# Performance work log

Measured on AMD Instinct MI355X. Metric: run time of the kernel, lower is better.

## Reference

```python
import jax, jax.numpy as jnp
import numpy as np

N = 50000
E = 800000
F_IN = 128
HEADS = 8
HID = 16
CLASSES = 40
NEG_SLOPE = 0.2


def setup_inputs() -> dict:
    key = jax.random.key(0)
    ks = jax.random.split(key, 10)
    return {
        "x": jax.random.normal(ks[0], (N, F_IN), jnp.float32),
        "edge_index": jax.random.randint(ks[1], (2, E), 0, N, jnp.int64),
        "W1": jax.random.normal(ks[2], (F_IN, HEADS * HID), jnp.float32) * 0.1,
        "a_src1": jax.random.normal(ks[3], (HEADS, HID), jnp.float32) * 0.1,
        "a_dst1": jax.random.normal(ks[4], (HEADS, HID), jnp.float32) * 0.1,
        "b1": jax.random.normal(ks[5], (HEADS * HID,), jnp.float32) * 0.1,
        "W2": jax.random.normal(ks[6], (HEADS * HID, CLASSES), jnp.float32) * 0.1,
        "a_src2": jax.random.normal(ks[7], (1, CLASSES), jnp.float32) * 0.1,
        "a_dst2": jax.random.normal(ks[8], (1, CLASSES), jnp.float32) * 0.1,
        "b2": jax.random.normal(ks[9], (CLASSES,), jnp.float32) * 0.1,
    }


def gat_conv(x, src, dst, W, a_src, a_dst, bias, heads, out_ch, concat):
    # x: [N, in] -> h: [N, H, C]
    h = (x @ W).reshape(N, heads, out_ch)
    e_src = jnp.einsum("nhc,hc->nh", h, a_src)  # [N, H]
    e_dst = jnp.einsum("nhc,hc->nh", h, a_dst)
    alpha = e_src[src] + e_dst[dst]             # [E, H]
    alpha = jax.nn.leaky_relu(alpha, NEG_SLOPE)
    # segment softmax over incoming edges of each dst node
    amax = jax.ops.segment_max(alpha, dst, num_segments=N)
    alpha = jnp.exp(alpha - amax[dst])
    denom = jax.ops.segment_sum(alpha, dst, num_segments=N)
    alpha = alpha / (denom[dst] + 1e-16)
    msg = h[src] * alpha[:, :, None]            # [E, H, C]
    out = jax.ops.segment_sum(msg, dst, num_segments=N)  # [N, H, C]
    out = out.reshape(N, heads * out_ch) if concat else out.mean(axis=1)
    return out + bias


def reference(x, edge_index, W1, a_src1, a_dst1, b1, W2, a_src2, a_dst2, b2):
    # PyG GATConv adds self-loops by default
    loops = jnp.arange(N, dtype=edge_index.dtype)
    src = jnp.concatenate([edge_index[0], loops])
    dst = jnp.concatenate([edge_index[1], loops])
    # inference: dropout layers are identity
    h = gat_conv(x, src, dst, W1, a_src1, a_dst1, b1, HEADS, HID, concat=True)
    h = jax.nn.elu(h)
    out = gat_conv(h, src, dst, W2, a_src2, a_dst2, b2, 1, CLASSES, concat=False)
    return out
```

## Files before the change

kernel.cpp:

```cpp
#include <hip/hip_runtime.h>
#include <math.h>

#define NN 50000
#define EE 800000
#define ET (EE + NN)
#define F_IN 128
#define HEADS 8
#define HID 16
#define C1 (HEADS * HID)
#define CLASSES 40
#define NEG_SLOPE 0.2f
#define LOG2E 1.4426950408889634f

#define NCHUNKS ((NN + 1023) / 1024)
#define NHIST 64
#define EPB (EE / NHIST)
#define LHN 25088
#define GB ((NN + 63) / 64)

typedef __attribute__((ext_vector_type(8))) short bf16x8;
typedef __attribute__((ext_vector_type(4))) float f32x4;
typedef __attribute__((ext_vector_type(8))) _Float16 h16x8;
typedef __attribute__((ext_vector_type(2))) _Float16 h16x2;

__device__ __forceinline__ unsigned cvtpk(float a, float b) {
    unsigned r;
    asm("v_cvt_pk_bf16_f32 %0, %1, %2" : "=v"(r) : "v"(a), "v"(b));
    return r;
}
__device__ __forceinline__ float fexp2(float x) {
    float r;
    asm("v_exp_f32 %0, %1\n\ts_nop 0" : "=v"(r) : "v"(x));
    return r;
}
__device__ __forceinline__ float bflo(unsigned u) { return __uint_as_float(u << 16); }
__device__ __forceinline__ float bfhi(unsigned u) { return __uint_as_float(u & 0xffff0000u); }
__device__ __forceinline__ float lrelu(float a) { return fmaxf(a, NEG_SLOPE * a); }
__device__ __forceinline__ unsigned short bf1(float a) { return (unsigned short)cvtpk(a, a); }
__device__ __forceinline__ float bf1f(float a) { return bflo(cvtpk(a, a)); }
__device__ __forceinline__ bf16x8 pack8(float f0, float f1, float f2, float f3,
                                        float f4, float f5, float f6, float f7) {
    union { unsigned u[4]; bf16x8 v; } U;
    U.u[0] = cvtpk(f0, f1);
    U.u[1] = cvtpk(f2, f3);
    U.u[2] = cvtpk(f4, f5);
    U.u[3] = cvtpk(f6, f7);
    return U.v;
}

__global__ void prep_kernel(const float* __restrict__ W1,
                            const float* __restrict__ as1, const float* __restrict__ ad1,
                            const float* __restrict__ W2,
                            const float* __restrict__ as2, const float* __restrict__ ad2,
                            const int* __restrict__ ei,
                            unsigned short* __restrict__ va1h, unsigned short* __restrict__ va1l,
                            unsigned short* __restrict__ va2b,
                            unsigned short* __restrict__ W1b, unsigned short* __restrict__ W2b,
                            unsigned* __restrict__ partial) {
    const int tid = threadIdx.x;
    const int b = blockIdx.x;
    if (b >= 3) {
        __shared__ unsigned lhist[LHN];
        for (int i = tid; i < LHN; i += 256) lhist[i] = 0;
        __syncthreads();
        const int hb = b - 3;
        const int* dp = ei + EE + hb * EPB;
        for (int e0 = tid * 4; e0 < EPB; e0 += 1024) {
            int4 d4 = *(const int4*)(dp + e0);
            atomicAdd(&lhist[(unsigned)d4.x >> 1], 1u << ((d4.x & 1) << 4));
            atomicAdd(&lhist[(unsigned)d4.y >> 1], 1u << ((d4.y & 1) << 4));
            atomicAdd(&lhist[(unsigned)d4.z >> 1], 1u << ((d4.z & 1) << 4));
            atomicAdd(&lhist[(unsigned)d4.w >> 1], 1u << ((d4.w & 1) << 4));
        }
        __syncthreads();
        unsigned* pb = partial + (size_t)hb * LHN;
        for (int i = tid; i < LHN; i += 256) pb[i] = lhist[i];
        return;
    }
    if (b == 1) {
        for (int f = tid; f < 2048; f += 256) {
            const int lane = f & 63, kc = (f >> 6) & 3, ntw = f >> 8;
            const int q = lane >> 4, c = lane & 15;
            const int col = ntw * 16 + c;
            const int k0 = kc * 32 + q * 8;
            const float* wp = W1 + (size_t)k0 * C1 + col;
            *(bf16x8*)(W1b + (size_t)f * 8) =
                pack8(wp[0], wp[C1], wp[2 * C1], wp[3 * C1],
                      wp[4 * C1], wp[5 * C1], wp[6 * C1], wp[7 * C1]);
        }
        return;
    }
    if (b == 2) {
        for (int f = tid; f < 768; f += 256) {
            const int lane = f & 63, kc = (f >> 6) & 3, nt = f >> 8;
            const int q = lane >> 4, c = lane & 15;
            const int col = nt * 16 + c;
            const int k0 = kc * 32 + q * 8;
            bf16x8 v = 0;
            if (col < CLASSES) {
                const float* wp = W2 + (size_t)k0 * CLASSES + col;
                v = pack8(wp[0], wp[CLASSES], wp[2 * CLASSES], wp[3 * CLASSES],
                          wp[4 * CLASSES], wp[5 * CLASSES], wp[6 * CLASSES], wp[7 * CLASSES]);
            }
            *(bf16x8*)(W2b + (size_t)f * 8) = v;
        }
        return;
    }
    {
        const int k = tid >> 1, half = tid & 1;
        const float* wrow = W1 + (size_t)k * C1 + half * 64;
        #pragma unroll
        for (int hh = 0; hh < 4; ++hh) {
            const int h = half * 4 + hh;
            float s = 0.f, d = 0.f;
            #pragma unroll
            for (int t = 0; t < 16; ++t) {
                float wv = wrow[hh * 16 + t];
                s += wv * as1[h * HID + t];
                d += wv * ad1[h * HID + t];
            }
            s *= LOG2E; d *= LOG2E;
            va1h[h * 128 + k]       = bf1(s);
            va1l[h * 128 + k]       = bf1(s - bf1f(s));
            va1h[(h + 8) * 128 + k] = bf1(d);
            va1l[(h + 8) * 128 + k] = bf1(d - bf1f(d));
        }
    }
    if (tid < C1) {
        const float* wrow = W2 + (size_t)tid * CLASSES;
        float s = 0.f, d = 0.f;
        #pragma unroll
        for (int c2 = 0; c2 < CLASSES; ++c2) {
            float wv = wrow[c2];
            s += wv * as2[c2];
            d += wv * ad2[c2];
        }
        s *= LOG2E; d *= LOG2E;
        va2b[0 * 128 + tid] = bf1(s);
        va2b[1 * 128 + tid] = bf1(s - bf1f(s));
        va2b[2 * 128 + tid] = bf1(d);
        va2b[3 * 128 + tid] = bf1(d - bf1f(d));
    }
}

__global__ void scan1_kernel(const unsigned* __restrict__ partial, int* __restrict__ deg,
                             int* __restrict__ rowptr, int* __restrict__ bsum) {
    __shared__ int sh[256];
    const int tid = threadIdx.x;
    const int base = blockIdx.x * 1024 + tid * 4;
    const unsigned short* pu = (const unsigned short*)partial;
    int t0 = 0, t1 = 0, t2 = 0, t3 = 0;
    #pragma unroll 8
    for (int b = 0; b < NHIST; ++b) {
        ushort4 p = *(const ushort4*)(pu + (size_t)b * (LHN * 2) + base);
        t0 += p.x; t1 += p.y; t2 += p.z; t3 += p.w;
    }
    int v[4], s[4];
    v[0] = (base + 0 < NN) ? t0 + 1 : 0;
    v[1] = (base + 1 < NN) ? t1 + 1 : 0;
    v[2] = (base + 2 < NN) ? t2 + 1 : 0;
    v[3] = (base + 3 < NN) ? t3 + 1 : 0;
    #pragma unroll
    for (int j = 0; j < 4; ++j)
        if (base + j < NN) deg[base + j] = v[j];
    s[0] = v[0]; s[1] = s[0] + v[1]; s[2] = s[1] + v[2]; s[3] = s[2] + v[3];
    int T = s[3];
    sh[tid] = T;
    __syncthreads();
    for (int off = 1; off < 256; off <<= 1) {
        int xv = (tid >= off) ? sh[tid - off] : 0;
        __syncthreads();
        sh[tid] += xv;
        __syncthreads();
    }
    int excl = sh[tid] - T;
    #pragma unroll
    for (int j = 0; j < 4; ++j)
        if (base + j < NN) rowptr[base + j] = excl + s[j] - v[j];
    if (tid == 255) bsum[blockIdx.x] = sh[255];
}

__global__ void scan3_kernel(int* __restrict__ rowptr, const int* __restrict__ bsum,
                             int* __restrict__ cursor, unsigned short* __restrict__ csr) {
    __shared__ int ex[64];
    const int tid = threadIdx.x;
    if (tid < 64) {
        int v = (tid < NCHUNKS) ? bsum[tid] : 0;
        int s = v;
        #pragma unroll
        for (int off = 1; off < 64; off <<= 1) {
            int xv = __shfl_up(s, off);
            if (tid >= off) s += xv;
        }
        ex[tid] = s - v;
    }
    __syncthreads();
    int i = blockIdx.x * blockDim.x + tid;
    if (i >= NN) return;
    int rp = rowptr[i] + ex[i >> 10];
    rowptr[i] = rp;
    cursor[i] = rp + 1;
    csr[rp] = (unsigned short)i;
}

__global__ __launch_bounds__(256, 4)
void gemm1_fill_kernel(const float* __restrict__ x,
                       const unsigned short* __restrict__ W1b,
                       const unsigned short* __restrict__ va1h,
                       const unsigned short* __restrict__ va1l,
                       const int* __restrict__ ei,
                       int* __restrict__ cursor, unsigned short* __restrict__ csr,
                       _Float16* __restrict__ h1h,
                       float* __restrict__ e_src, float* __restrict__ e_dst) {
    const int bid = blockIdx.x;
    const int tid = threadIdx.x;
    if (bid & 1) {
        int base = ((bid >> 1) * 256 + tid) * 4;
        if (base < EE) {
            int4 s4 = *(const int4*)(ei + base);
            int4 d4 = *(const int4*)(ei + EE + base);
            int p0 = atomicAdd(&cursor[d4.x], 1);
            int p1 = atomicAdd(&cursor[d4.y], 1);
            int p2 = atomicAdd(&cursor[d4.z], 1);
            int p3 = atomicAdd(&cursor[d4.w], 1);
            csr[p0] = (unsigned short)s4.x;
            csr[p1] = (unsigned short)s4.y;
            csr[p2] = (unsigned short)s4.z;
            csr[p3] = (unsigned short)s4.w;
        }
        return;
    }
    const int gemmb = bid >> 1;
    const int w = tid >> 6, lane = tid & 63;
    const int q = lane >> 4, c = lane & 15;
    const int m0 = (gemmb * 4 + w) * 16;

    int row = m0 + c;
    if (row > NN - 1) row = NN - 1;
    bf16x8 afrag[4];
    #pragma unroll
    for (int kc = 0; kc < 4; ++kc) {
        const float* xp = x + (size_t)row * F_IN + kc * 32 + q * 8;
        float4 p0 = *(const float4*)xp;
        float4 p1 = *(const float4*)(xp + 4);
        afrag[kc] = pack8(p0.x, p0.y, p0.z, p0.w, p1.x, p1.y, p1.z, p1.w);
    }

    {
        f32x4 acce = {0.f, 0.f, 0.f, 0.f};
        #pragma unroll
        for (int kc = 0; kc < 4; ++kc) {
            const int coloff = kc * 32 + q * 8;
            bf16x8 beh = *(const bf16x8*)(va1h + c * 128 + coloff);
            bf16x8 bel = *(const bf16x8*)(va1l + c * 128 + coloff);
            acce = __builtin_amdgcn_mfma_f32_16x16x32_bf16(afrag[kc], beh, acce, 0, 0, 0);
            acce = __builtin_amdgcn_mfma_f32_16x16x32_bf16(afrag[kc], bel, acce, 0, 0, 0);
        }
        float* ep = (c < 8) ? e_src : e_dst;
        const int cc = c & 7;
        #pragma unroll
        for (int r = 0; r < 4; ++r) {
            const int ro = m0 + q * 4 + r;
            if (ro < NN) ep[(size_t)ro * HEADS + cc] = acce[r];
        }
    }

    #pragma unroll 2
    for (int nt = 0; nt < 8; ++nt) {
        bf16x8 bf0 = *(const bf16x8*)(W1b + (size_t)((nt * 4 + 0) * 64 + lane) * 8);
        bf16x8 bf1_ = *(const bf16x8*)(W1b + (size_t)((nt * 4 + 1) * 64 + lane) * 8);
        bf16x8 bf2 = *(const bf16x8*)(W1b + (size_t)((nt * 4 + 2) * 64 + lane) * 8);
        bf16x8 bf3 = *(const bf16x8*)(W1b + (size_t)((nt * 4 + 3) * 64 + lane) * 8);
        f32x4 a = {0.f, 0.f, 0.f, 0.f};
        a = __builtin_amdgcn_mfma_f32_16x16x32_bf16(afrag[0], bf0, a, 0, 0, 0);
        a = __builtin_amdgcn_mfma_f32_16x16x32_bf16(afrag[1], bf1_, a, 0, 0, 0);
        a = __builtin_amdgcn_mfma_f32_16x16x32_bf16(afrag[2], bf2, a, 0, 0, 0);
        a = __builtin_amdgcn_mfma_f32_16x16x32_bf16(afrag[3], bf3, a, 0, 0, 0);
        #pragma unroll
        for (int r = 0; r < 4; ++r) {
            const int ro = m0 + q * 4 + r;
            if (ro < NN) h1h[(size_t)ro * C1 + nt * 16 + c] = (_Float16)a[r];
        }
    }
}

__global__ __launch_bounds__(64)
void agg1_kernel(const _Float16* __restrict__ h1h,
                 const float* __restrict__ e_src, const float* __restrict__ e_dst,
                 const int* __restrict__ rowptr, const int* __restrict__ deg,
                 const unsigned short* __restrict__ csr,
                 const float* __restrict__ b1, unsigned short* __restrict__ hmid) {
    const int tid = threadIdx.x;
    const int l = tid & 15;
    const int d = blockIdx.x * 4 + (tid >> 4);
    const int hd = l >> 1;
    const float ed = e_dst[(size_t)d * HEADS + hd];
    const int start = rowptr[d];
    const int cnt = deg[d];

    float denom = 0.f;
    float acc[8] = {0.f, 0.f, 0.f, 0.f, 0.f, 0.f, 0.f, 0.f};

    for (int i = 0; i < cnt; i += 8) {
        int s[8];
        #pragma unroll
        for (int e = 0; e < 8; ++e)
            s[e] = csr[start + ((i + e < cnt) ? i + e : i)];
        float es[8];
        #pragma unroll
        for (int e = 0; e < 8; ++e)
            es[e] = e_src[(size_t)s[e] * HEADS + hd];
        h16x8 g[8];
        #pragma unroll
        for (int e = 0; e < 8; ++e)
            g[e] = *(const h16x8*)(h1h + (size_t)s[e] * C1 + 8 * l);
        float w[8];
        #pragma unroll
        for (int e = 0; e < 8; ++e) {
            float we = fexp2(lrelu(es[e] + ed));
            w[e] = (i + e < cnt) ? we : 0.f;
            denom += w[e];
        }
        #pragma unroll
        for (int e = 0; e < 8; ++e) {
            #pragma unroll
            for (int j = 0; j < 8; ++j)
                acc[j] = fmaf((float)g[e][j], w[e], acc[j]);
        }
    }
    const float inv = 1.f / (denom + 1e-16f);
    float o[8];
    #pragma unroll
    for (int k = 0; k < 8; ++k) {
        float t = acc[k] * inv + b1[8 * l + k];
        o[k] = (t > 0.f) ? t : fexp2(t * LOG2E) - 1.f;
    }
    uint4 st;
    st.x = cvtpk(o[0], o[1]);
    st.y = cvtpk(o[2], o[3]);
    st.z = cvtpk(o[4], o[5]);
    st.w = cvtpk(o[6], o[7]);
    *(uint4*)(hmid + (size_t)d * C1 + 8 * l) = st;
}

__global__ __launch_bounds__(256, 4)
void gemm2_kernel(const unsigned short* __restrict__ hmid,
                  const unsigned short* __restrict__ W2b,
                  const unsigned short* __restrict__ va2b,
                  _Float16* __restrict__ h2h,
                  float* __restrict__ e_src, float* __restrict__ e_dst) {
    const int tid = threadIdx.x;
    const int w = tid >> 6, lane = tid & 63;
    const int q = lane >> 4, c = lane & 15;

    const int m0 = (blockIdx.x * 4 + w) * 16;
    if (m0 >= NN) return;
    int row = m0 + c;
    if (row > NN - 1) row = NN - 1;
    bf16x8 afrag[4];
    #pragma unroll
    for (int kc = 0; kc < 4; ++kc)
        afrag[kc] = *(const bf16x8*)(hmid + (size_t)row * C1 + kc * 32 + q * 8);

    bf16x8 bfrag[3][4];
    #pragma unroll
    for (int nt = 0; nt < 3; ++nt)
        #pragma unroll
        for (int kc = 0; kc < 4; ++kc)
            bfrag[nt][kc] = *(const bf16x8*)(W2b + (size_t)((nt * 4 + kc) * 64 + lane) * 8);
    bf16x8 bfe[4];
    #pragma unroll
    for (int kc = 0; kc < 4; ++kc) {
        bf16x8 bb = 0;
        if (c < 4) bb = *(const bf16x8*)(va2b + c * 128 + kc * 32 + q * 8);
        bfe[kc] = bb;
    }

    f32x4 acc[3] = {{0.f,0.f,0.f,0.f},{0.f,0.f,0.f,0.f},{0.f,0.f,0.f,0.f}};
    f32x4 acce = {0.f, 0.f, 0.f, 0.f};
    #pragma unroll
    for (int kc = 0; kc < 4; ++kc) {
        acc[0] = __builtin_amdgcn_mfma_f32_16x16x32_bf16(afrag[kc], bfrag[0][kc], acc[0], 0, 0, 0);
        acc[1] = __builtin_amdgcn_mfma_f32_16x16x32_bf16(afrag[kc], bfrag[1][kc], acc[1], 0, 0, 0);
        acc[2] = __builtin_amdgcn_mfma_f32_16x16x32_bf16(afrag[kc], bfrag[2][kc], acc[2], 0, 0, 0);
        acce   = __builtin_amdgcn_mfma_f32_16x16x32_bf16(afrag[kc], bfe[kc],      acce,   0, 0, 0);
    }
    #pragma unroll
    for (int r = 0; r < 4; ++r) {
        const int ro = m0 + q * 4 + r;
        float v = acce[r] + __shfl_xor(acce[r], 1);
        if (ro < NN) {
            #pragma unroll
            for (int nt = 0; nt < 3; ++nt) {
                const int col = nt * 16 + c;
                if (col < CLASSES)
                    h2h[(size_t)ro * CLASSES + col] = (_Float16)acc[nt][r];
            }
            if (c == 0) e_src[ro] = v;
            if (c == 2) e_dst[ro] = v;
        }
    }
}

__global__ __launch_bounds__(64)
void agg2_kernel(const _Float16* __restrict__ h2h,
                 const float* __restrict__ e_src, const float* __restrict__ e_dst,
                 const int* __restrict__ rowptr, const int* __restrict__ deg,
                 const unsigned short* __restrict__ csr,
                 const float* __restrict__ b2, float* __restrict__ out) {
    const int tid = threadIdx.x;
    const int eg = tid / 20;
    const int c  = tid % 20;
    const int d = blockIdx.x * 3 + eg;
    const bool live = (eg < 3) && (d < NN);
    const int dcl = live ? d : 0;
    const float ed = e_dst[dcl];
    const int start = rowptr[dcl];
    const int cnt = live ? deg[dcl] : 0;

    float denom = 0.f, acc0 = 0.f, acc1 = 0.f;
    for (int i = 0; i < cnt; i += 8) {
        int s[8];
        #pragma unroll
        for (int e = 0; e < 8; ++e)
            s[e] = csr[start + ((i + e < cnt) ? i + e : i)];
        float es[8];
        #pragma unroll
        for (int e = 0; e < 8; ++e)
            es[e] = e_src[s[e]];
        h16x2 g[8];
        #pragma unroll
        for (int e = 0; e < 8; ++e)
            g[e] = *(const h16x2*)(h2h + (size_t)s[e] * CLASSES + 2 * c);
        float w[8];
        #pragma unroll
        for (int e = 0; e < 8; ++e) {
            float we = fexp2(lrelu(es[e] + ed));
            w[e] = (i + e < cnt) ? we : 0.f;
            denom += w[e];
        }
        #pragma unroll
        for (int e = 0; e < 8; ++e) {
            acc0 = fmaf((float)g[e][0], w[e], acc0);
            acc1 = fmaf((float)g[e][1], w[e], acc1);
        }
    }
    if (live) {
        const float inv = 1.f / (denom + 1e-16f);
        float2 o;
        o.x = acc0 * inv + b2[2 * c];
        o.y = acc1 * inv + b2[2 * c + 1];
        *(float2*)(out + (size_t)d * CLASSES + 2 * c) = o;
    }
}

extern "C" void kernel_launch(void* const* d_in, const int* in_sizes, int n_in,
                              void* d_out, int out_size, void* d_ws, size_t ws_size,
                              hipStream_t stream) {
    const float* x      = (const float*)d_in[0];
    const int*   ei     = (const int*)d_in[1];
    const float* W1     = (const float*)d_in[2];
    const float* a_src1 = (const float*)d_in[3];
    const float* a_dst1 = (const float*)d_in[4];
    const float* b1     = (const float*)d_in[5];
    const float* W2     = (const float*)d_in[6];
    const float* a_src2 = (const float*)d_in[7];
    const float* a_dst2 = (const float*)d_in[8];
    const float* b2     = (const float*)d_in[9];
    float* out = (float*)d_out;

    char* ws = (char*)d_ws;
    size_t off = 0;
    auto alloc = [&](size_t bytes) { char* p = ws + off; off += (bytes + 255) & ~(size_t)255; return p; };
    _Float16* h1h = (_Float16*)alloc((size_t)NN * C1 * 2);
    _Float16* h2h = (_Float16*)alloc((size_t)NN * CLASSES * 2);
    unsigned short* hmidb = (unsigned short*)alloc((size_t)NN * C1 * 2);
    float* e_src1 = (float*)alloc((size_t)NN * HEADS * 4);
    float* e_dst1 = (float*)alloc((size_t)NN * HEADS * 4);
    float* e_src2 = (float*)alloc((size_t)NN * 4);
    float* e_dst2 = (float*)alloc((size_t)NN * 4);
    int*   deg    = (int*)alloc((size_t)NN * 4);
    int*   rowptr = (int*)alloc((size_t)NN * 4);
    int*   cursor = (int*)alloc((size_t)NN * 4);
    unsigned short* csr  = (unsigned short*)alloc((size_t)ET * 2);
    int*   bsum   = (int*)alloc(256 * 4);
    unsigned short* va1h = (unsigned short*)alloc(16 * 128 * 2);
    unsigned short* va1l = (unsigned short*)alloc(16 * 128 * 2);
    unsigned short* va2b = (unsigned short*)alloc(4 * 128 * 2);
    unsigned short* W1b  = (unsigned short*)alloc(2048 * 8 * 2);
    unsigned short* W2b  = (unsigned short*)alloc(768 * 8 * 2);
    unsigned* partial    = (unsigned*)alloc((size_t)NHIST * LHN * 4);

    prep_kernel<<<3 + NHIST, 256, 0, stream>>>(W1, a_src1, a_dst1, W2, a_src2, a_dst2, ei,
                                               va1h, va1l, va2b, W1b, W2b, partial);
    scan1_kernel<<<NCHUNKS, 256, 0, stream>>>(partial, deg, rowptr, bsum);
    scan3_kernel<<<(NN + 255) / 256, 256, 0, stream>>>(rowptr, bsum, cursor, csr);
    gemm1_fill_kernel<<<2 * GB, 256, 0, stream>>>(x, W1b, va1h, va1l, ei, cursor, csr,
                                                  h1h, e_src1, e_dst1);

    agg1_kernel<<<NN / 4, 64, 0, stream>>>(h1h, e_src1, e_dst1, rowptr, deg, csr, b1, hmidb);

    gemm2_kernel<<<(NN + 63) / 64, 256, 0, stream>>>(hmidb, W2b, va2b, h2h, e_src2, e_dst2);
    agg2_kernel<<<(NN + 2) / 3, 64, 0, stream>>>(h2h, e_src2, e_dst2, rowptr, deg, csr, b2, out);
}
```

Baseline: 217.4 us.

## Replace global-atomic CSR fill with per-block LDS ranking and byte prefix offsets

The destination histogram now uses 8-bit counters packed four per word in LDS, and the scan kernel also writes a per-histogram-block exclusive prefix in bytes. The CSR fill is redone by the same 64 edge partitions, each ranking its edges with LDS atomics and placing them at rowptr plus prefix plus local rank. This removes the global atomic cursor array and its contention. The cost is an extra prefix buffer, a big LDS allocation in the fused GEMM kernel (occupancy hint lowered to 3), and 8-bit counters that could overflow if one node receives 256 or more edges within a single partition.

```diff
diff --git a/kernel.cpp b/kernel.cpp
--- a/kernel.cpp
+++ b/kernel.cpp
@@ -15,7 +15,8 @@
 #define NCHUNKS ((NN + 1023) / 1024)
 #define NHIST 64
 #define EPB (EE / NHIST)
-#define LHN 25088
+#define PADN (NCHUNKS * 1024)
+#define LDSW (PADN / 4)
 #define GB ((NN + 63) / 64)
 
 typedef __attribute__((ext_vector_type(8))) short bf16x8;
@@ -56,25 +57,25 @@
                             unsigned short* __restrict__ va1h, unsigned short* __restrict__ va1l,
                             unsigned short* __restrict__ va2b,
                             unsigned short* __restrict__ W1b, unsigned short* __restrict__ W2b,
-                            unsigned* __restrict__ partial) {
+                            unsigned char* __restrict__ partial8) {
     const int tid = threadIdx.x;
     const int b = blockIdx.x;
     if (b >= 3) {
-        __shared__ unsigned lhist[LHN];
-        for (int i = tid; i < LHN; i += 256) lhist[i] = 0;
+        __shared__ unsigned lhist[LDSW];
+        for (int i = tid; i < LDSW; i += 256) lhist[i] = 0;
         __syncthreads();
         const int hb = b - 3;
         const int* dp = ei + EE + hb * EPB;
         for (int e0 = tid * 4; e0 < EPB; e0 += 1024) {
             int4 d4 = *(const int4*)(dp + e0);
-            atomicAdd(&lhist[(unsigned)d4.x >> 1], 1u << ((d4.x & 1) << 4));
-            atomicAdd(&lhist[(unsigned)d4.y >> 1], 1u << ((d4.y & 1) << 4));
-            atomicAdd(&lhist[(unsigned)d4.z >> 1], 1u << ((d4.z & 1) << 4));
-            atomicAdd(&lhist[(unsigned)d4.w >> 1], 1u << ((d4.w & 1) << 4));
+            atomicAdd(&lhist[(unsigned)d4.x >> 2], 1u << (((unsigned)d4.x & 3) << 3));
+            atomicAdd(&lhist[(unsigned)d4.y >> 2], 1u << (((unsigned)d4.y & 3) << 3));
+            atomicAdd(&lhist[(unsigned)d4.z >> 2], 1u << (((unsigned)d4.z & 3) << 3));
+            atomicAdd(&lhist[(unsigned)d4.w >> 2], 1u << (((unsigned)d4.w & 3) << 3));
         }
         __syncthreads();
-        unsigned* pb = partial + (size_t)hb * LHN;
-        for (int i = tid; i < LHN; i += 256) pb[i] = lhist[i];
+        unsigned* pb = (unsigned*)(partial8 + (size_t)hb * PADN);
+        for (int i = tid; i < LDSW; i += 256) pb[i] = lhist[i];
         return;
     }
     if (b == 1) {
@@ -143,16 +144,21 @@
     }
 }
 
-__global__ void scan1_kernel(const unsigned* __restrict__ partial, int* __restrict__ deg,
+__global__ void scan1_kernel(const unsigned char* __restrict__ partial8,
+                             unsigned char* __restrict__ pfx8,
+                             int* __restrict__ deg,
                              int* __restrict__ rowptr, int* __restrict__ bsum) {
     __shared__ int sh[256];
     const int tid = threadIdx.x;
     const int base = blockIdx.x * 1024 + tid * 4;
-    const unsigned short* pu = (const unsigned short*)partial;
     int t0 = 0, t1 = 0, t2 = 0, t3 = 0;
     #pragma unroll 8
     for (int b = 0; b < NHIST; ++b) {
-        ushort4 p = *(const ushort4*)(pu + (size_t)b * (LHN * 2) + base);
+        uchar4 pf;
+        pf.x = (unsigned char)t0; pf.y = (unsigned char)t1;
+        pf.z = (unsigned char)t2; pf.w = (unsigned char)t3;
+        *(uchar4*)(pfx8 + (size_t)b * PADN + base) = pf;
+        uchar4 p = *(const uchar4*)(partial8 + (size_t)b * PADN + base);
         t0 += p.x; t1 += p.y; t2 += p.z; t3 += p.w;
     }
     int v[4], s[4];
@@ -181,7 +187,7 @@
 }
 
 __global__ void scan3_kernel(int* __restrict__ rowptr, const int* __restrict__ bsum,
-                             int* __restrict__ cursor, unsigned short* __restrict__ csr) {
+                             unsigned short* __restrict__ csr) {
     __shared__ int ex[64];
     const int tid = threadIdx.x;
     if (tid < 64) {
@@ -199,38 +205,57 @@
     if (i >= NN) return;
     int rp = rowptr[i] + ex[i >> 10];
     rowptr[i] = rp;
-    cursor[i] = rp + 1;
     csr[rp] = (unsigned short)i;
 }
 
-__global__ __launch_bounds__(256, 4)
+__global__ __launch_bounds__(256, 3)
 void gemm1_fill_kernel(const float* __restrict__ x,
                        const unsigned short* __restrict__ W1b,
                        const unsigned short* __restrict__ va1h,
                        const unsigned short* __restrict__ va1l,
                        const int* __restrict__ ei,
-                       int* __restrict__ cursor, unsigned short* __restrict__ csr,
+                       const int* __restrict__ rowptr,
+                       const unsigned char* __restrict__ pfx8,
+                       unsigned short* __restrict__ csr,
                        _Float16* __restrict__ h1h,
                        float* __restrict__ e_src, float* __restrict__ e_dst) {
     const int bid = blockIdx.x;
     const int tid = threadIdx.x;
-    if (bid & 1) {
-        int base = ((bid >> 1) * 256 + tid) * 4;
-        if (base < EE) {
-            int4 s4 = *(const int4*)(ei + base);
-            int4 d4 = *(const int4*)(ei + EE + base);
-            int p0 = atomicAdd(&cursor[d4.x], 1);
-            int p1 = atomicAdd(&cursor[d4.y], 1);
-            int p2 = atomicAdd(&cursor[d4.z], 1);
-            int p3 = atomicAdd(&cursor[d4.w], 1);
-            csr[p0] = (unsigned short)s4.x;
-            csr[p1] = (unsigned short)s4.y;
-            csr[p2] = (unsigned short)s4.z;
-            csr[p3] = (unsigned short)s4.w;
+    __shared__ unsigned lrank[LDSW];
+    if (bid < NHIST) {
+        for (int i = tid; i < LDSW; i += 256) lrank[i] = 0;
+        __syncthreads();
+        const int fb = bid;
+        const int* sp = ei + fb * EPB;
+        const int* dp = ei + EE + fb * EPB;
+        const unsigned char* pf = pfx8 + (size_t)fb * PADN;
+        for (int e0 = tid * 4; e0 < EPB; e0 += 1024) {
+            int4 s4 = *(const int4*)(sp + e0);
+            int4 d4 = *(const int4*)(dp + e0);
+            {
+                const unsigned d = (unsigned)d4.x, sh8 = (d & 3) << 3;
+                unsigned old = atomicAdd(&lrank[d >> 2], 1u << sh8);
+                csr[rowptr[d] + 1 + pf[d] + ((old >> sh8) & 0xff)] = (unsigned short)s4.x;
+            }
+            {
+                const unsigned d = (unsigned)d4.y, sh8 = (d & 3) << 3;
+                unsigned old = atomicAdd(&lrank[d >> 2], 1u << sh8);
+                csr[rowptr[d] + 1 + pf[d] + ((old >> sh8) & 0xff)] = (unsigned short)s4.y;
+            }
+            {
+                const unsigned d = (unsigned)d4.z, sh8 = (d & 3) << 3;
+                unsigned old = atomicAdd(&lrank[d >> 2], 1u << sh8);
+                csr[rowptr[d] + 1 + pf[d] + ((old >> sh8) & 0xff)] = (unsigned short)s4.z;
+            }
+            {
+                const unsigned d = (unsigned)d4.w, sh8 = (d & 3) << 3;
+                unsigned old = atomicAdd(&lrank[d >> 2], 1u << sh8);
+                csr[rowptr[d] + 1 + pf[d] + ((old >> sh8) & 0xff)] = (unsigned short)s4.w;
+            }
         }
         return;
     }
-    const int gemmb = bid >> 1;
+    const int gemmb = bid - NHIST;
     const int w = tid >> 6, lane = tid & 63;
     const int q = lane >> 4, c = lane & 15;
     const int m0 = (gemmb * 4 + w) * 16;
@@ -481,7 +506,6 @@
     float* e_dst2 = (float*)alloc((size_t)NN * 4);
     int*   deg    = (int*)alloc((size_t)NN * 4);
     int*   rowptr = (int*)alloc((size_t)NN * 4);
-    int*   cursor = (int*)alloc((size_t)NN * 4);
     unsigned short* csr  = (unsigned short*)alloc((size_t)ET * 2);
     int*   bsum   = (int*)alloc(256 * 4);
     unsigned short* va1h = (unsigned short*)alloc(16 * 128 * 2);
@@ -489,14 +513,15 @@
     unsigned short* va2b = (unsigned short*)alloc(4 * 128 * 2);
     unsigned short* W1b  = (unsigned short*)alloc(2048 * 8 * 2);
     unsigned short* W2b  = (unsigned short*)alloc(768 * 8 * 2);
-    unsigned* partial    = (unsigned*)alloc((size_t)NHIST * LHN * 4);
+    unsigned char* partial8 = (unsigned char*)alloc((size_t)NHIST * PADN);
+    unsigned char* pfx8     = (unsigned char*)alloc((size_t)NHIST * PADN);
 
     prep_kernel<<<3 + NHIST, 256, 0, stream>>>(W1, a_src1, a_dst1, W2, a_src2, a_dst2, ei,
-                                               va1h, va1l, va2b, W1b, W2b, partial);
-    scan1_kernel<<<NCHUNKS, 256, 0, stream>>>(partial, deg, rowptr, bsum);
-    scan3_kernel<<<(NN + 255) / 256, 256, 0, stream>>>(rowptr, bsum, cursor, csr);
-    gemm1_fill_kernel<<<2 * GB, 256, 0, stream>>>(x, W1b, va1h, va1l, ei, cursor, csr,
-                                                  h1h, e_src1, e_dst1);
+                                               va1h, va1l, va2b, W1b, W2b, partial8);
+    scan1_kernel<<<NCHUNKS, 256, 0, stream>>>(partial8, pfx8, deg, rowptr, bsum);
+    scan3_kernel<<<(NN + 255) / 256, 256, 0, stream>>>(rowptr, bsum, csr);
+    gemm1_fill_kernel<<<NHIST + GB, 256, 0, stream>>>(x, W1b, va1h, va1l, ei, rowptr, pfx8,
+                                                      csr, h1h, e_src1, e_dst1);
 
     agg1_kernel<<<NN / 4, 64, 0, stream>>>(h1h, e_src1, e_dst1, rowptr, deg, csr, b1, hmidb);
 
```

New measurement: 206.1 us. 5.2% less time.
